# Optimization experiments

Measured on AMD Instinct MI355X. Metric: run time of the kernel, lower is better.

The kernel has to match this reference:

```python
import jax, jax.numpy as jnp
import numpy as np

NUM_NODES = 100000
NUM_EDGES = 640000


def setup_inputs() -> dict:
    key = jax.random.key(0)
    ks = jax.random.split(key, 6)
    x = jax.random.normal(ks[0], (NUM_NODES, 128), dtype=jnp.float32)
    edge_index = jax.random.randint(ks[1], (2, NUM_EDGES), 0, NUM_NODES, dtype=jnp.int64)
    s1 = 1.0 / np.sqrt(128.0)
    s2 = 1.0 / np.sqrt(128.0)
    return {
        "x": x,
        "edge_index": edge_index,
        "W1_l": jax.random.normal(ks[2], (128, 128), dtype=jnp.float32) * s1,
        "b1": jnp.zeros((128,), dtype=jnp.float32),
        "W1_r": jax.random.normal(ks[3], (128, 128), dtype=jnp.float32) * s1,
        "W2_l": jax.random.normal(ks[4], (128, 64), dtype=jnp.float32) * s2,
        "b2": jnp.zeros((64,), dtype=jnp.float32),
        "W2_r": jax.random.normal(ks[5], (128, 64), dtype=jnp.float32) * s2,
    }


def _sage_conv(x, src, dst, Wl, b, Wr, num_nodes):
    # PyG SAGEConv (mean aggr): out = lin_l(mean_{j in N(i)} x_j) + lin_r(x_i)
    msg = x[src]                                                    # [E, d] gather
    agg = jax.ops.segment_sum(msg, dst, num_segments=num_nodes)     # [N, d]
    deg = jax.ops.segment_sum(jnp.ones((dst.shape[0],), x.dtype), dst,
                              num_segments=num_nodes)               # [N]
    mean = agg / jnp.maximum(deg, 1.0)[:, None]
    return mean @ Wl + b + x @ Wr


def reference(x, edge_index, W1_l, b1, W1_r, W2_l, b2, W2_r):
    num_nodes = x.shape[0]
    src, dst = edge_index[0], edge_index[1]
    h = jax.nn.relu(_sage_conv(x, src, dst, W1_l, b1, W1_r, num_nodes))
    # F.dropout(p=0.5) is identity in eval mode
    out = _sage_conv(h, src, dst, W2_l, b2, W2_r, num_nodes)
    return out
```

## Files before the change

### kernel.cpp

```cpp
#include <hip/hip_runtime.h>
#include <hip/hip_bf16.h>


#define NNODES 100000
#define NEDGES 640000

typedef __attribute__((ext_vector_type(8))) short short8v;
typedef __attribute__((ext_vector_type(4))) float f32x4;
typedef unsigned int uint;
typedef unsigned short ushort;

__device__ __forceinline__ float b2f(ushort u) {
    return __uint_as_float(((uint)u) << 16);
}
__device__ __forceinline__ ushort f2b(float f) {
    uint u = __float_as_uint(f);
    return (ushort)((u + 0x7fffu + ((u >> 16) & 1u)) >> 16);
}


__global__ void hist_kernel(const int* __restrict__ dst, int* __restrict__ count, int E) {
    int e = blockIdx.x * blockDim.x + threadIdx.x;
    if (e < E) atomicAdd(&count[dst[e]], 1);
}

__global__ void block_sum_kernel(const int* __restrict__ count, int* __restrict__ bsum, int N) {
    __shared__ int s[256];
    int t = threadIdx.x;
    int i = blockIdx.x * 256 + t;
    s[t] = (i < N) ? count[i] : 0;
    __syncthreads();
    for (int off = 128; off > 0; off >>= 1) {
        if (t < off) s[t] += s[t + off];
        __syncthreads();
    }
    if (t == 0) bsum[blockIdx.x] = s[0];
}

__global__ void scan_bsum_kernel(int* __restrict__ bsum, int nb) {
    __shared__ int s[512];
    int t = threadIdx.x;
    int orig = (t < nb) ? bsum[t] : 0;
    s[t] = orig;
    __syncthreads();
    for (int off = 1; off < 512; off <<= 1) {
        int v = (t >= off) ? s[t - off] : 0;
        __syncthreads();
        s[t] += v;
        __syncthreads();
    }
    if (t < nb) bsum[t] = s[t] - orig;
}

__global__ void scan_write_kernel(const int* __restrict__ count, const int* __restrict__ bsum,
                                  int* __restrict__ rp, int N, int E) {
    __shared__ int s[256];
    int t = threadIdx.x;
    int i = blockIdx.x * 256 + t;
    int orig = (i < N) ? count[i] : 0;
    s[t] = orig;
    __syncthreads();
    for (int off = 1; off < 256; off <<= 1) {
        int v = (t >= off) ? s[t - off] : 0;
        __syncthreads();
        s[t] += v;
        __syncthreads();
    }
    if (i < N) rp[i] = bsum[blockIdx.x] + s[t] - orig;
    if (i == 0) rp[N] = E;
}

__global__ void bucket_kernel(const int* __restrict__ src, const int* __restrict__ dst,
                              const int* __restrict__ rp, int* __restrict__ cursor,
                              int* __restrict__ esrc, int E) {
    int e = blockIdx.x * blockDim.x + threadIdx.x;
    if (e >= E) return;
    int d = dst[e];
    int pos = atomicAdd(&cursor[d], 1);
    esrc[rp[d] + pos] = src[e];
}


__global__ __launch_bounds__(256)
void cast_x_kernel(const float* __restrict__ x, ushort* __restrict__ xb,
                   ushort* __restrict__ A1, int N) {
    int i = blockIdx.x * 256 + threadIdx.x;
    if (i >= N * 16) return;
    int n = i >> 4, c8 = (i & 15) * 8;
    const float* px = x + (size_t)n * 128 + c8;
    float4 v0 = *reinterpret_cast<const float4*>(px);
    float4 v1 = *reinterpret_cast<const float4*>(px + 4);
    ushort o[8];
    o[0] = f2b(v0.x); o[1] = f2b(v0.y); o[2] = f2b(v0.z); o[3] = f2b(v0.w);
    o[4] = f2b(v1.x); o[5] = f2b(v1.y); o[6] = f2b(v1.z); o[7] = f2b(v1.w);
    short8v vv = *reinterpret_cast<short8v*>(o);
    *reinterpret_cast<short8v*>(xb + (size_t)n * 128 + c8) = vv;
    *reinterpret_cast<short8v*>(A1 + (size_t)n * 256 + 128 + c8) = vv;
}

__global__ __launch_bounds__(256)
void cast_w_kernel(const float* __restrict__ P0, const float* __restrict__ P1,
                   ushort* __restrict__ Wc, int K, int mode) {
    int u = blockIdx.x * 256 + threadIdx.x;
    if (u >= K * 16) return;
    int t = u >> 9;
    int g = (u >> 6) & 7;
    int l = u & 63;
    int k0 = t * 32 + ((l >> 4) * 8);
    int c = g * 16 + (l & 15);
    ushort o[8];
    #pragma unroll
    for (int j = 0; j < 8; ++j) {
        int k = k0 + j;
        float v;
        if (mode == 0) v = (k < 128) ? P0[k * 128 + c] : P1[(k - 128) * 128 + c];
        else           v = (c < 64)  ? P0[k * 64 + c]  : P1[k * 64 + (c - 64)];
        o[j] = f2b(v);
    }
    *reinterpret_cast<short8v*>(Wc + (size_t)u * 8) = *reinterpret_cast<short8v*>(o);
}


__global__ __launch_bounds__(256)
void gather_mean_bf16(const ushort* __restrict__ xb, const int* __restrict__ rp,
                      const int* __restrict__ esrc, ushort* __restrict__ A1, int N) {
    int gid = blockIdx.x * 256 + threadIdx.x;
    int n = gid >> 4, lane = gid & 15;
    if (n >= N) return;
    int beg = rp[n], end = rp[n + 1];
    float acc[8] = {0.f, 0.f, 0.f, 0.f, 0.f, 0.f, 0.f, 0.f};
    int j = beg;
    for (; j + 2 <= end; j += 2) {
        int s0 = esrc[j], s1 = esrc[j + 1];
        short8v v0 = *reinterpret_cast<const short8v*>(xb + (size_t)s0 * 128 + lane * 8);
        short8v v1 = *reinterpret_cast<const short8v*>(xb + (size_t)s1 * 128 + lane * 8);
        #pragma unroll
        for (int i = 0; i < 8; ++i) acc[i] += b2f((ushort)v0[i]) + b2f((ushort)v1[i]);
    }
    if (j < end) {
        int s0 = esrc[j];
        short8v v0 = *reinterpret_cast<const short8v*>(xb + (size_t)s0 * 128 + lane * 8);
        #pragma unroll
        for (int i = 0; i < 8; ++i) acc[i] += b2f((ushort)v0[i]);
    }
    float inv = 1.0f / fmaxf((float)(end - beg), 1.0f);
    ushort o[8];
    #pragma unroll
    for (int i = 0; i < 8; ++i) o[i] = f2b(acc[i] * inv);
    *reinterpret_cast<short8v*>(A1 + (size_t)n * 256 + lane * 8) = *reinterpret_cast<short8v*>(o);
}

__global__ __launch_bounds__(256)
void gather_out64_bf16(const ushort* __restrict__ q, const int* __restrict__ rp,
                       const int* __restrict__ esrc, float* __restrict__ out, int N) {
    int gid = blockIdx.x * 256 + threadIdx.x;
    int n = gid >> 3, lane = gid & 7;
    if (n >= N) return;
    int beg = rp[n], end = rp[n + 1];
    float acc[8] = {0.f, 0.f, 0.f, 0.f, 0.f, 0.f, 0.f, 0.f};
    int j = beg;
    for (; j + 2 <= end; j += 2) {
        int s0 = esrc[j], s1 = esrc[j + 1];
        short8v v0 = *reinterpret_cast<const short8v*>(q + (size_t)s0 * 128 + lane * 8);
        short8v v1 = *reinterpret_cast<const short8v*>(q + (size_t)s1 * 128 + lane * 8);
        #pragma unroll
        for (int i = 0; i < 8; ++i) acc[i] += b2f((ushort)v0[i]) + b2f((ushort)v1[i]);
    }
    if (j < end) {
        int s0 = esrc[j];
        short8v v0 = *reinterpret_cast<const short8v*>(q + (size_t)s0 * 128 + lane * 8);
        #pragma unroll
        for (int i = 0; i < 8; ++i) acc[i] += b2f((ushort)v0[i]);
    }
    float inv = 1.0f / fmaxf((float)(end - beg), 1.0f);
    short8v sv = *reinterpret_cast<const short8v*>(q + (size_t)n * 128 + 64 + lane * 8);
    float o[8];
    #pragma unroll
    for (int i = 0; i < 8; ++i) o[i] = acc[i] * inv + b2f((ushort)sv[i]);
    float* po = out + (size_t)n * 64 + lane * 8;
    *reinterpret_cast<float4*>(po)     = make_float4(o[0], o[1], o[2], o[3]);
    *reinterpret_cast<float4*>(po + 4) = make_float4(o[4], o[5], o[6], o[7]);
}

template<int K, int BMODE, bool RELU>
__global__ __launch_bounds__(256)
void mfma_gemm_kernel(const ushort* __restrict__ A, const ushort* __restrict__ Wc,
                      const float* __restrict__ bias, ushort* __restrict__ C, int N)
{
    __shared__ ushort cbuf[4][32][128];
    const int wid = threadIdx.x >> 6;
    const int l = threadIdx.x & 63;
    const int row0 = blockIdx.x * 128 + wid * 32;
    const int ar = l & 15;
    const int ak = (l >> 4) * 8;

    f32x4 zz = {0.f, 0.f, 0.f, 0.f};
    f32x4 acc[2][8];
    #pragma unroll
    for (int g = 0; g < 8; ++g) { acc[0][g] = zz; acc[1][g] = zz; }

    const int rA0 = row0 + ar;
    const int rA1 = row0 + 16 + ar;
    const bool v0 = rA0 < N, v1 = rA1 < N;
    const ushort* a0p = A + (size_t)rA0 * K + ak;
    const ushort* a1p = A + (size_t)rA1 * K + ak;
    const short8v* wbase = reinterpret_cast<const short8v*>(Wc);
    short8v az = {0, 0, 0, 0, 0, 0, 0, 0};

    #pragma unroll
    for (int t = 0; t < K / 32; ++t) {
        short8v af0 = az, af1 = az;
        if (v0) af0 = *reinterpret_cast<const short8v*>(a0p + t * 32);
        if (v1) af1 = *reinterpret_cast<const short8v*>(a1p + t * 32);
        const short8v* wf = wbase + (size_t)(t * 8) * 64 + l;
        #pragma unroll
        for (int g = 0; g < 8; ++g) {
            short8v bf = wf[g * 64];
            acc[0][g] = __builtin_amdgcn_mfma_f32_16x16x32_bf16(af0, bf, acc[0][g], 0, 0, 0);
            acc[1][g] = __builtin_amdgcn_mfma_f32_16x16x32_bf16(af1, bf, acc[1][g], 0, 0, 0);
        }
    }

    const int cr4 = (l >> 4) * 4;
    const int cc = l & 15;
    #pragma unroll
    for (int g = 0; g < 8; ++g) {
        int col = g * 16 + cc;
        float bv = (BMODE == 0) ? bias[col] : ((col >= 64) ? bias[col - 64] : 0.f);
        #pragma unroll
        for (int j = 0; j < 4; ++j) {
            float u0 = acc[0][g][j] + bv;
            float u1 = acc[1][g][j] + bv;
            if (RELU) { u0 = fmaxf(u0, 0.f); u1 = fmaxf(u1, 0.f); }
            cbuf[wid][cr4 + j][col]      = f2b(u0);
            cbuf[wid][16 + cr4 + j][col] = f2b(u1);
        }
    }
    __syncthreads();

    const ushort* cf = &cbuf[wid][0][0];
    #pragma unroll
    for (int p = 0; p < 8; ++p) {
        int idx = p * 64 + l;
        int fr = idx >> 4;
        int r = row0 + fr;
        if (r < N)
            *reinterpret_cast<short8v*>(C + (size_t)r * 128 + (idx & 15) * 8) =
                *reinterpret_cast<const short8v*>(cf + idx * 8);
    }
}


extern "C" void kernel_launch(void* const* d_in, const int* in_sizes, int n_in,
                              void* d_out, int out_size, void* d_ws, size_t ws_size,
                              hipStream_t stream)
{
    const float* x   = (const float*)d_in[0];
    const int*   ei  = (const int*)d_in[1];
    const float* W1l = (const float*)d_in[2];
    const float* b1  = (const float*)d_in[3];
    const float* W1r = (const float*)d_in[4];
    const float* W2l = (const float*)d_in[5];
    const float* b2  = (const float*)d_in[6];
    const float* W2r = (const float*)d_in[7];
    float* out = (float*)d_out;

    const int N = NNODES, E = NEDGES;
    const int* src = ei;
    const int* dst = ei + E;

    char* ws = (char*)d_ws;
    int* count  = (int*)ws;
    int* cursor = count + N;
    int* rp     = cursor + N;
    int* bsum   = rp + N + 1;
    int* esrc   = bsum + 512;
    const size_t MB = 1024u * 1024u;
    ushort* Wc1 = (ushort*)(ws + 4 * MB);
    ushort* Wc2 = (ushort*)(ws + 4 * MB + 64 * 1024);
    ushort* A1  = (ushort*)(ws + 4 * MB + 128 * 1024);
    ushort* xb  = A1 + (size_t)N * 256;
    ushort* h = xb;
    ushort* q = A1;

    const int nb = (N + 255) / 256;

    hipMemsetAsync(ws, 0, (size_t)2 * N * 4, stream);

    hist_kernel<<<(E + 255) / 256, 256, 0, stream>>>(dst, count, E);
    block_sum_kernel<<<nb, 256, 0, stream>>>(count, bsum, N);
    scan_bsum_kernel<<<1, 512, 0, stream>>>(bsum, nb);
    scan_write_kernel<<<nb, 256, 0, stream>>>(count, bsum, rp, N, E);
    bucket_kernel<<<(E + 255) / 256, 256, 0, stream>>>(src, dst, rp, cursor, esrc, E);

    cast_x_kernel<<<(N * 16 + 255) / 256, 256, 0, stream>>>(x, xb, A1, N);
    cast_w_kernel<<<(256 * 16 + 255) / 256, 256, 0, stream>>>(W1l, W1r, Wc1, 256, 0);
    cast_w_kernel<<<(128 * 16 + 255) / 256, 256, 0, stream>>>(W2l, W2r, Wc2, 128, 1);

    gather_mean_bf16<<<(N * 16 + 255) / 256, 256, 0, stream>>>(xb, rp, esrc, A1, N);
    mfma_gemm_kernel<256, 0, true><<<(N + 127) / 128, 256, 0, stream>>>(A1, Wc1, b1, h, N);

    mfma_gemm_kernel<128, 1, false><<<(N + 127) / 128, 256, 0, stream>>>(h, Wc2, b2, q, N);
    gather_out64_bf16<<<(N * 8 + 255) / 256, 256, 0, stream>>>(q, rp, esrc, out, N);
}
```

Measured before the change: 269.4 us.

## Fuse prep kernels into one launch and fuse both layer GEMMs via LDS

Merges the degree histogram, x cast and both weight casts into a single prep kernel to cut launch count. The two MFMA GEMMs are fused: the ReLU hidden activations stay in padded shared memory and feed the second GEMM directly, so h is never written to or read back from global memory. This saves one launch and a full N×128 bf16 round-trip. In exchange it raises LDS use per block for the padded buffer and makes the prep kernel heavier.

```diff
diff --git a/kernel.cpp b/kernel.cpp
--- a/kernel.cpp
+++ b/kernel.cpp
@@ -18,11 +18,6 @@
     return (ushort)((u + 0x7fffu + ((u >> 16) & 1u)) >> 16);
 }
 
-
-__global__ void hist_kernel(const int* __restrict__ dst, int* __restrict__ count, int E) {
-    int e = blockIdx.x * blockDim.x + threadIdx.x;
-    if (e < E) atomicAdd(&count[dst[e]], 1);
-}
 
 __global__ void block_sum_kernel(const int* __restrict__ count, int* __restrict__ bsum, int N) {
     __shared__ int s[256];
@@ -80,44 +75,57 @@
     esrc[rp[d] + pos] = src[e];
 }
 
-
 __global__ __launch_bounds__(256)
-void cast_x_kernel(const float* __restrict__ x, ushort* __restrict__ xb,
-                   ushort* __restrict__ A1, int N) {
+void prep_kernel(const float* __restrict__ x, ushort* __restrict__ xb, ushort* __restrict__ A1,
+                 const int* __restrict__ dst, int* __restrict__ count,
+                 const float* __restrict__ W1l, const float* __restrict__ W1r, ushort* __restrict__ Wc1,
+                 const float* __restrict__ W2l, const float* __restrict__ W2r, ushort* __restrict__ Wc2,
+                 int N, int E)
+{
     int i = blockIdx.x * 256 + threadIdx.x;
-    if (i >= N * 16) return;
-    int n = i >> 4, c8 = (i & 15) * 8;
-    const float* px = x + (size_t)n * 128 + c8;
-    float4 v0 = *reinterpret_cast<const float4*>(px);
-    float4 v1 = *reinterpret_cast<const float4*>(px + 4);
-    ushort o[8];
-    o[0] = f2b(v0.x); o[1] = f2b(v0.y); o[2] = f2b(v0.z); o[3] = f2b(v0.w);
-    o[4] = f2b(v1.x); o[5] = f2b(v1.y); o[6] = f2b(v1.z); o[7] = f2b(v1.w);
-    short8v vv = *reinterpret_cast<short8v*>(o);
-    *reinterpret_cast<short8v*>(xb + (size_t)n * 128 + c8) = vv;
-    *reinterpret_cast<short8v*>(A1 + (size_t)n * 256 + 128 + c8) = vv;
-}
-
-__global__ __launch_bounds__(256)
-void cast_w_kernel(const float* __restrict__ P0, const float* __restrict__ P1,
-                   ushort* __restrict__ Wc, int K, int mode) {
-    int u = blockIdx.x * 256 + threadIdx.x;
-    if (u >= K * 16) return;
-    int t = u >> 9;
-    int g = (u >> 6) & 7;
-    int l = u & 63;
-    int k0 = t * 32 + ((l >> 4) * 8);
-    int c = g * 16 + (l & 15);
-    ushort o[8];
-    #pragma unroll
-    for (int j = 0; j < 8; ++j) {
-        int k = k0 + j;
-        float v;
-        if (mode == 0) v = (k < 128) ? P0[k * 128 + c] : P1[(k - 128) * 128 + c];
-        else           v = (c < 64)  ? P0[k * 64 + c]  : P1[k * 64 + (c - 64)];
-        o[j] = f2b(v);
-    }
-    *reinterpret_cast<short8v*>(Wc + (size_t)u * 8) = *reinterpret_cast<short8v*>(o);
+
+    if (i < N * 16) {
+        int n = i >> 4, c8 = (i & 15) * 8;
+        const float* px = x + (size_t)n * 128 + c8;
+        float4 v0 = *reinterpret_cast<const float4*>(px);
+        float4 v1 = *reinterpret_cast<const float4*>(px + 4);
+        ushort o[8];
+        o[0] = f2b(v0.x); o[1] = f2b(v0.y); o[2] = f2b(v0.z); o[3] = f2b(v0.w);
+        o[4] = f2b(v1.x); o[5] = f2b(v1.y); o[6] = f2b(v1.z); o[7] = f2b(v1.w);
+        short8v vv = *reinterpret_cast<short8v*>(o);
+        *reinterpret_cast<short8v*>(xb + (size_t)n * 128 + c8) = vv;
+        *reinterpret_cast<short8v*>(A1 + (size_t)n * 256 + 128 + c8) = vv;
+    }
+
+    if (i < E) atomicAdd(&count[dst[i]], 1);
+
+    if (i < 256 * 16) {
+        int u = i;
+        int t = u >> 9, g = (u >> 6) & 7, l = u & 63;
+        int k0 = t * 32 + ((l >> 4) * 8);
+        int c = g * 16 + (l & 15);
+        ushort o[8];
+        #pragma unroll
+        for (int j = 0; j < 8; ++j) {
+            int k = k0 + j;
+            float v = (k < 128) ? W1l[k * 128 + c] : W1r[(k - 128) * 128 + c];
+            o[j] = f2b(v);
+        }
+        *reinterpret_cast<short8v*>(Wc1 + (size_t)u * 8) = *reinterpret_cast<short8v*>(o);
+    } else if (i < 256 * 16 + 128 * 16) {
+        int u = i - 256 * 16;
+        int t = u >> 9, g = (u >> 6) & 7, l = u & 63;
+        int k0 = t * 32 + ((l >> 4) * 8);
+        int c = g * 16 + (l & 15);
+        ushort o[8];
+        #pragma unroll
+        for (int j = 0; j < 8; ++j) {
+            int k = k0 + j;
+            float v = (c < 64) ? W2l[k * 64 + c] : W2r[k * 64 + (c - 64)];
+            o[j] = f2b(v);
+        }
+        *reinterpret_cast<short8v*>(Wc2 + (size_t)u * 8) = *reinterpret_cast<short8v*>(o);
+    }
 }
 
 
@@ -182,12 +190,12 @@
     *reinterpret_cast<float4*>(po + 4) = make_float4(o[4], o[5], o[6], o[7]);
 }
 
-template<int K, int BMODE, bool RELU>
 __global__ __launch_bounds__(256)
-void mfma_gemm_kernel(const ushort* __restrict__ A, const ushort* __restrict__ Wc,
-                      const float* __restrict__ bias, ushort* __restrict__ C, int N)
+void fused_gemm_kernel(const ushort* __restrict__ A1, const ushort* __restrict__ Wc1,
+                       const float* __restrict__ b1, const ushort* __restrict__ Wc2,
+                       const float* __restrict__ b2, ushort* __restrict__ q, int N)
 {
-    __shared__ ushort cbuf[4][32][128];
+    __shared__ ushort hbuf[4][32][136];
     const int wid = threadIdx.x >> 6;
     const int l = threadIdx.x & 63;
     const int row0 = blockIdx.x * 128 + wid * 32;
@@ -199,54 +207,86 @@
     #pragma unroll
     for (int g = 0; g < 8; ++g) { acc[0][g] = zz; acc[1][g] = zz; }
 
-    const int rA0 = row0 + ar;
-    const int rA1 = row0 + 16 + ar;
-    const bool v0 = rA0 < N, v1 = rA1 < N;
-    const ushort* a0p = A + (size_t)rA0 * K + ak;
-    const ushort* a1p = A + (size_t)rA1 * K + ak;
-    const short8v* wbase = reinterpret_cast<const short8v*>(Wc);
-    short8v az = {0, 0, 0, 0, 0, 0, 0, 0};
-
-    #pragma unroll
-    for (int t = 0; t < K / 32; ++t) {
-        short8v af0 = az, af1 = az;
-        if (v0) af0 = *reinterpret_cast<const short8v*>(a0p + t * 32);
-        if (v1) af1 = *reinterpret_cast<const short8v*>(a1p + t * 32);
-        const short8v* wf = wbase + (size_t)(t * 8) * 64 + l;
+    {
+        const int rA0 = row0 + ar;
+        const int rA1 = row0 + 16 + ar;
+        const bool v0 = rA0 < N, v1 = rA1 < N;
+        const ushort* a0p = A1 + (size_t)rA0 * 256 + ak;
+        const ushort* a1p = A1 + (size_t)rA1 * 256 + ak;
+        const short8v* wbase = reinterpret_cast<const short8v*>(Wc1);
+        short8v az = {0, 0, 0, 0, 0, 0, 0, 0};
+        #pragma unroll
+        for (int t = 0; t < 8; ++t) {
+            short8v af0 = az, af1 = az;
+            if (v0) af0 = *reinterpret_cast<const short8v*>(a0p + t * 32);
+            if (v1) af1 = *reinterpret_cast<const short8v*>(a1p + t * 32);
+            const short8v* wf = wbase + (size_t)(t * 8) * 64 + l;
+            #pragma unroll
+            for (int g = 0; g < 8; ++g) {
+                short8v bf = wf[g * 64];
+                acc[0][g] = __builtin_amdgcn_mfma_f32_16x16x32_bf16(af0, bf, acc[0][g], 0, 0, 0);
+                acc[1][g] = __builtin_amdgcn_mfma_f32_16x16x32_bf16(af1, bf, acc[1][g], 0, 0, 0);
+            }
+        }
+    }
+
+    {
+        const int cr4 = (l >> 4) * 4;
+        const int cc = l & 15;
         #pragma unroll
         for (int g = 0; g < 8; ++g) {
-            short8v bf = wf[g * 64];
-            acc[0][g] = __builtin_amdgcn_mfma_f32_16x16x32_bf16(af0, bf, acc[0][g], 0, 0, 0);
-            acc[1][g] = __builtin_amdgcn_mfma_f32_16x16x32_bf16(af1, bf, acc[1][g], 0, 0, 0);
-        }
-    }
-
-    const int cr4 = (l >> 4) * 4;
-    const int cc = l & 15;
-    #pragma unroll
-    for (int g = 0; g < 8; ++g) {
-        int col = g * 16 + cc;
-        float bv = (BMODE == 0) ? bias[col] : ((col >= 64) ? bias[col - 64] : 0.f);
-        #pragma unroll
-        for (int j = 0; j < 4; ++j) {
-            float u0 = acc[0][g][j] + bv;
-            float u1 = acc[1][g][j] + bv;
-            if (RELU) { u0 = fmaxf(u0, 0.f); u1 = fmaxf(u1, 0.f); }
-            cbuf[wid][cr4 + j][col]      = f2b(u0);
-            cbuf[wid][16 + cr4 + j][col] = f2b(u1);
-        }
-    }
-    __syncthreads();
-
-    const ushort* cf = &cbuf[wid][0][0];
+            int col = g * 16 + cc;
+            float bv = b1[col];
+            #pragma unroll
+            for (int j = 0; j < 4; ++j) {
+                hbuf[wid][cr4 + j][col]      = f2b(fmaxf(acc[0][g][j] + bv, 0.f));
+                hbuf[wid][16 + cr4 + j][col] = f2b(fmaxf(acc[1][g][j] + bv, 0.f));
+            }
+        }
+    }
+
+    #pragma unroll
+    for (int g = 0; g < 8; ++g) { acc[0][g] = zz; acc[1][g] = zz; }
+    {
+        const short8v* wbase = reinterpret_cast<const short8v*>(Wc2);
+        #pragma unroll
+        for (int t = 0; t < 4; ++t) {
+            short8v af0 = *reinterpret_cast<const short8v*>(&hbuf[wid][ar][t * 32 + ak]);
+            short8v af1 = *reinterpret_cast<const short8v*>(&hbuf[wid][16 + ar][t * 32 + ak]);
+            const short8v* wf = wbase + (size_t)(t * 8) * 64 + l;
+            #pragma unroll
+            for (int g = 0; g < 8; ++g) {
+                short8v bf = wf[g * 64];
+                acc[0][g] = __builtin_amdgcn_mfma_f32_16x16x32_bf16(af0, bf, acc[0][g], 0, 0, 0);
+                acc[1][g] = __builtin_amdgcn_mfma_f32_16x16x32_bf16(af1, bf, acc[1][g], 0, 0, 0);
+            }
+        }
+    }
+
+    {
+        const int cr4 = (l >> 4) * 4;
+        const int cc = l & 15;
+        #pragma unroll
+        for (int g = 0; g < 8; ++g) {
+            int col = g * 16 + cc;
+            float bv = (col >= 64) ? b2[col - 64] : 0.f;
+            #pragma unroll
+            for (int j = 0; j < 4; ++j) {
+                hbuf[wid][cr4 + j][col]      = f2b(acc[0][g][j] + bv);
+                hbuf[wid][16 + cr4 + j][col] = f2b(acc[1][g][j] + bv);
+            }
+        }
+    }
+
     #pragma unroll
     for (int p = 0; p < 8; ++p) {
         int idx = p * 64 + l;
         int fr = idx >> 4;
+        int c8 = idx & 15;
         int r = row0 + fr;
         if (r < N)
-            *reinterpret_cast<short8v*>(C + (size_t)r * 128 + (idx & 15) * 8) =
-                *reinterpret_cast<const short8v*>(cf + idx * 8);
+            *reinterpret_cast<short8v*>(q + (size_t)r * 128 + c8 * 8) =
+                *reinterpret_cast<const short8v*>(&hbuf[wid][fr][c8 * 8]);
     }
 }
 
@@ -280,26 +320,22 @@
     ushort* Wc2 = (ushort*)(ws + 4 * MB + 64 * 1024);
     ushort* A1  = (ushort*)(ws + 4 * MB + 128 * 1024);
     ushort* xb  = A1 + (size_t)N * 256;
-    ushort* h = xb;
-    ushort* q = A1;
+    ushort* q   = xb + (size_t)N * 128;
 
     const int nb = (N + 255) / 256;
 
     hipMemsetAsync(ws, 0, (size_t)2 * N * 4, stream);
 
-    hist_kernel<<<(E + 255) / 256, 256, 0, stream>>>(dst, count, E);
+    prep_kernel<<<(N * 16 + 255) / 256, 256, 0, stream>>>(
+        x, xb, A1, dst, count, W1l, W1r, Wc1, W2l, W2r, Wc2, N, E);
+
     block_sum_kernel<<<nb, 256, 0, stream>>>(count, bsum, N);
     scan_bsum_kernel<<<1, 512, 0, stream>>>(bsum, nb);
     scan_write_kernel<<<nb, 256, 0, stream>>>(count, bsum, rp, N, E);
     bucket_kernel<<<(E + 255) / 256, 256, 0, stream>>>(src, dst, rp, cursor, esrc, E);
 
-    cast_x_kernel<<<(N * 16 + 255) / 256, 256, 0, stream>>>(x, xb, A1, N);
-    cast_w_kernel<<<(256 * 16 + 255) / 256, 256, 0, stream>>>(W1l, W1r, Wc1, 256, 0);
-    cast_w_kernel<<<(128 * 16 + 255) / 256, 256, 0, stream>>>(W2l, W2r, Wc2, 128, 1);
-
     gather_mean_bf16<<<(N * 16 + 255) / 256, 256, 0, stream>>>(xb, rp, esrc, A1, N);
-    mfma_gemm_kernel<256, 0, true><<<(N + 127) / 128, 256, 0, stream>>>(A1, Wc1, b1, h, N);
-
-    mfma_gemm_kernel<128, 1, false><<<(N + 127) / 128, 256, 0, stream>>>(h, Wc2, b2, q, N);
+    fused_gemm_kernel<<<(N + 127) / 128, 256, 0, stream>>>(A1, Wc1, b1, Wc2, b2, q, N);
+
     gather_out64_bf16<<<(N * 8 + 255) / 256, 256, 0, stream>>>(q, rp, esrc, out, N);
 }
```

After: 263.0 us. 2.4% less time.
